# Optimization experiments

Hardware: AMD Instinct MI355X
Metric: run time of the kernel (lower is better)

The kernel has to match this reference:

```python
import jax, jax.numpy as jnp
import numpy as np

B, N, M, D = 2, 8192, 8192, 2
CIN, COUT, E, K = 32, 32, 16, 32
GAMMA = float(E * E)  # RBF sharpness
MUS = jnp.linspace(0.0, 1.0, E)  # RBF centers on [0, 1] (points drawn from unit square)


def setup_inputs() -> dict:
    key = jax.random.key(0)
    k1, k2, k3, k4, k5 = jax.random.split(key, 5)
    points_in = jax.random.uniform(k1, (B, N, D), dtype=jnp.float32)
    values_in = jax.random.normal(k2, (B, N, CIN), dtype=jnp.float32)
    points_out = jax.random.uniform(k3, (B, M, D), dtype=jnp.float32)
    coeff = jax.random.normal(k4, (CIN, COUT, E), dtype=jnp.float32)
    bias = jax.random.normal(k5, (COUT,), dtype=jnp.float32)
    return {"points_in": points_in, "values_in": values_in, "points_out": points_out,
            "coeff": coeff, "bias": bias}


def reference(points_in, values_in, points_out, coeff, bias):
    # u_inverse_v = g(points_out)^{-1} applied to points_in; for the translation
    # group this is the pairwise relative position tensor. Torch computes it
    # under no_grad -> stop_gradient here.
    uiv = points_out[:, :, None, :] - points_in[:, None, :, :]        # [B, M, N, D]
    norms = jnp.linalg.norm(uiv, axis=-1)                              # [B, M, N]
    neg_r, idx = jax.lax.top_k(-norms, K)                              # smallest K dists
    r_k = jax.lax.stop_gradient(-neg_r)                                # [B, M, K]
    idx = jax.lax.stop_gradient(idx)                                   # [B, M, K] int32
    uiv_k = jax.lax.stop_gradient(
        jnp.take_along_axis(uiv, idx[..., None], axis=2))              # [B, M, K, D]
    # det == 1 for translation group (non-Tensor in torch -> branch skipped)
    # gather neighbor values: values_in broadcast over M, gathered along N
    vals_k = jnp.take_along_axis(values_in[:, None, :, :], idx[..., None], axis=2)  # [B, M, K, CIN]
    # Gaussian radial kernel basis evaluated on |u_inverse_v|
    kernel_b = jnp.exp(-GAMMA * (r_k[..., None] - MUS) ** 2)           # [B, M, K, E]
    out = jnp.einsum('ioe,bmke,bmki->bmo', coeff, kernel_b, vals_k) / K
    out = out + bias
    return uiv_k, idx, out
```

## Files before the change

### kernel.cpp

```cpp
#include <hip/hip_runtime.h>
#include <cstdint>
#include <cstddef>

constexpr int BB   = 2;
constexpr int NN   = 8192;
constexpr int MM   = 8192;
constexpr int CIN  = 32;
constexpr int COUT = 32;
constexpr int EE   = 16;
constexpr int KK   = 32;
constexpr int GRID = 32;
constexpr int NCELL = GRID * GRID;

#define QPB 4
#define QPB2 8
#define CAP 128
#define KEY_BYTES 1040
#define VROW 36
#define VQS  1156
#define ECH 4

#define R0_FAST 0.0432f

constexpr size_t OFS_COEFFT = 0;
constexpr size_t OFS_COUNTS = 65536;
constexpr size_t OFS_CURSOR = 73728;
constexpr size_t OFS_STARTS = 81920;
constexpr size_t OFS_PTSS   = 90624;
constexpr size_t OFS_IDXS   = 221696;

__global__ __launch_bounds__(256) void prep_coeff_zero(const float* __restrict__ coeff,
                                                       float* __restrict__ coeff2,
                                                       int* __restrict__ cz) {
    int tid = blockIdx.x * 256 + threadIdx.x;
    if (tid < 2 * 2 * NCELL) cz[tid] = 0;
    if (tid >= EE * CIN * COUT) return;
    int o = tid & 31;
    int i = (tid >> 5) & 31;
    int e = tid >> 10;
    coeff2[tid] = coeff[(i * COUT + o) * EE + e];
}

__device__ __forceinline__ int cell_of(float2 p) {
    int cx = min(GRID - 1, max(0, (int)(p.x * (float)GRID)));
    int cy = min(GRID - 1, max(0, (int)(p.y * (float)GRID)));
    return cy * GRID + cx;
}

__global__ __launch_bounds__(256) void bin_count(const float* __restrict__ pts,
                                                 int* __restrict__ counts) {
    int t = blockIdx.x * 256 + threadIdx.x;
    int b = t >> 13, i = t & (NN - 1);
    float2 p = ((const float2*)pts)[(size_t)b * NN + i];
    atomicAdd(&counts[b * NCELL + cell_of(p)], 1);
}

__global__ __launch_bounds__(1024) void bin_scan(const int* __restrict__ counts,
                                                 int* __restrict__ starts) {
    __shared__ int wsum[16];
    const int b    = blockIdx.x;
    const int t    = threadIdx.x;
    const int lane = t & 63, wv = t >> 6;
    int s = counts[b * NCELL + t];
#pragma unroll
    for (int off = 1; off < 64; off <<= 1) {
        const int v = __shfl_up(s, off, 64);
        if (lane >= off) s += v;
    }
    if (lane == 63) wsum[wv] = s;
    __syncthreads();
    if (wv == 0) {
        int ws = (lane < 16) ? wsum[lane] : 0;
#pragma unroll
        for (int off = 1; off < 16; off <<= 1) {
            const int v = __shfl_up(ws, off, 64);
            if (lane >= off) ws += v;
        }
        if (lane < 16) wsum[lane] = ws;
    }
    __syncthreads();
    const int woff = (wv > 0) ? wsum[wv - 1] : 0;
    starts[b * (NCELL + 1) + t + 1] = s + woff;
    if (t == 0) starts[b * (NCELL + 1)] = 0;
}

__global__ __launch_bounds__(256) void bin_scatter(const float* __restrict__ pts,
                                                   const int* __restrict__ starts,
                                                   int* __restrict__ cursor,
                                                   float2* __restrict__ pts_s,
                                                   int* __restrict__ idx_s) {
    int t = blockIdx.x * 256 + threadIdx.x;
    int b = t >> 13, i = t & (NN - 1);
    float2 p = ((const float2*)pts)[(size_t)b * NN + i];
    int cell = cell_of(p);
    int pos = starts[b * (NCELL + 1) + cell] + atomicAdd(&cursor[b * NCELL + cell], 1);
    pts_s[(size_t)b * NN + pos] = p;
    idx_s[(size_t)b * NN + pos] = i;
}

__global__ __launch_bounds__(128) void conv_knn(
    const float2* __restrict__ pts_s, const int* __restrict__ idx_s,
    const int* __restrict__ starts,
    const float* __restrict__ points_in,
    const float* __restrict__ points_out,
    float* __restrict__ out_uiv, float* __restrict__ out_idx)
{
    __shared__ alignas(16) unsigned char SMEM[QPB][KEY_BYTES];

    const int tid   = threadIdx.x;
    const int sl    = tid & 31;
    const int qslot = tid >> 5;
    const int half  = qslot & 1;
    const int wid   = blockIdx.x * QPB + qslot;
    const int b     = wid >> 13;
    const int m     = wid & (MM - 1);

    unsigned long long* KEYq = (unsigned long long*)&SMEM[qslot][0];

    const float2* PS = pts_s + (size_t)b * NN;
    const int*    IS = idx_s + (size_t)b * NN;
    const int*    ST = starts + b * (NCELL + 1);
    const float2* P  = ((const float2*)points_in) + (size_t)b * NN;
    const float2  q  = ((const float2*)points_out)[(size_t)b * MM + m];

    const float INF = __builtin_inff();
    const float h = 1.0f / (float)GRID;
    const unsigned lmlt32 = (1u << sl) - 1u;

    float bd;
    int   bi;
    bool  ok = false;

    {
        float tau = R0_FAST;
        {
            const float bx = fminf(q.x, 1.0f - q.x);
            const float by = fminf(q.y, 1.0f - q.y);
#pragma unroll
            for (int it = 0; it < 3; ++it) {
                const float wx = 0.5f + 0.5f * fminf(bx / tau, 1.0f);
                const float wy = 0.5f + 0.5f * fminf(by / tau, 1.0f);
                tau = R0_FAST * __frsqrt_rn(wx * wy);
            }
        }
        const float tau2  = tau * tau;
        const float tau2a = tau2 * (1.0f + 2e-6f);

        const int xlo = (int)fmaxf((q.x - tau) * (float)GRID, 0.0f);
        const int xhi = (int)fminf((q.x + tau) * (float)GRID, (float)(GRID - 1));
        const int ylo = (int)fmaxf((q.y - tau) * (float)GRID, 0.0f);
        const int yhi = (int)fminf((q.y + tau) * (float)GRID, (float)(GRID - 1));
        const int nrows = yhi - ylo + 1;

        int sv = 0, ev = 0;
        if (sl < nrows) {
            sv = ST[(ylo + sl) * GRID + xlo];
            ev = ST[(ylo + sl) * GRID + xhi + 1];
        }

        int base = 0, nin = 0;
        for (int r = 0; r < nrows; ++r) {
            const int s = __shfl(sv, r, 32), e = __shfl(ev, r, 32);
            for (int j0 = s; j0 < e; j0 += 32) {
                const int j = j0 + sl;
                const bool valid = (j < e);
                float2 p = make_float2(2.0f, 2.0f);
                if (valid) p = PS[j];
                const float dx = q.x - p.x, dy = q.y - p.y;
                const float d2 = __builtin_fmaf(dy, dy, __fmul_rn(dx, dx));
                const bool adm = valid && (d2 <= tau2a);
                const unsigned bmA = (unsigned)(__ballot(adm) >> (half << 5));
                const unsigned bmS = (unsigned)(__ballot(valid && (d2 <= tau2)) >> (half << 5));
                nin += __popc(bmS);
                if (bmA) {
                    const float ex = __fsqrt_rn(__fadd_rn(__fmul_rn(dx, dx),
                                                          __fmul_rn(dy, dy)));
                    const int pos = base + __popc(bmA & lmlt32);
                    if (adm && pos < CAP)
                        KEYq[pos] =
                            ((unsigned long long)__float_as_uint(ex) << 32) | (unsigned)IS[j];
                    base += __popc(bmA);
                }
            }
        }

        ok = (nin >= 32) && (base <= CAP);
        if (ok) {
            unsigned long long k0 = (sl      < base) ? KEYq[sl]      : ~0ull;
            unsigned long long k1 = (sl + 32 < base) ? KEYq[sl + 32] : ~0ull;
            int r0 = 0, r1 = 0;
            if (!__any(base > 64)) {
                for (int t = 0; t < base; ++t) {
                    const unsigned long long kt = KEYq[t];
                    r0 += (kt < k0) ? 1 : 0;
                    r1 += (kt < k1) ? 1 : 0;
                }
            } else {
                unsigned long long k2 = (sl + 64 < base) ? KEYq[sl + 64] : ~0ull;
                unsigned long long k3 = (sl + 96 < base) ? KEYq[sl + 96] : ~0ull;
                int r2 = 0, r3 = 0;
                for (int t = 0; t < base; ++t) {
                    const unsigned long long kt = KEYq[t];
                    r0 += (kt < k0) ? 1 : 0;
                    r1 += (kt < k1) ? 1 : 0;
                    r2 += (kt < k2) ? 1 : 0;
                    r3 += (kt < k3) ? 1 : 0;
                }
                if (sl + 64 < base && r2 < 32) KEYq[r2] = k2;
                if (sl + 96 < base && r3 < 32) KEYq[r3] = k3;
            }
            if (sl      < base && r0 < 32) KEYq[r0] = k0;
            if (sl + 32 < base && r1 < 32) KEYq[r1] = k1;
            const unsigned long long kf = KEYq[sl];
            bd = __uint_as_float((unsigned)(kf >> 32));
            bi = (int)(unsigned)(kf & 0xffffffffull);

            const float tau32 = __shfl(bd, 31, 32);
            float g = INF;
            if (xlo > 0)        g = fminf(g, q.x - (float)xlo * h);
            if (xhi < GRID - 1) g = fminf(g, (float)(xhi + 1) * h - q.x);
            if (ylo > 0)        g = fminf(g, q.y - (float)ylo * h);
            if (yhi < GRID - 1) g = fminf(g, (float)(yhi + 1) * h - q.y);
            ok = (tau32 < g * (1.0f - 4e-6f));
        }
    }

    if (!ok) {
        const int cx = min(GRID - 1, max(0, (int)(q.x * (float)GRID)));
        const int cy = min(GRID - 1, max(0, (int)(q.y * (float)GRID)));
        int L = 2;
        for (;;) {
            const int xlo = max(cx - L, 0), xhi = min(cx + L, GRID - 1);
            const int ylo = max(cy - L, 0), yhi = min(cy + L, GRID - 1);
            const int nrows = yhi - ylo + 1;

            int sv = 0, ev = 0;
            if (sl < nrows) {
                sv = ST[(ylo + sl) * GRID + xlo];
                ev = ST[(ylo + sl) * GRID + xhi + 1];
            }

            float mn1 = INF, mn2 = INF;
            for (int r = 0; r < nrows; ++r) {
                const int s = __shfl(sv, r, 32), e = __shfl(ev, r, 32);
                for (int j = s + sl; j < e; j += 32) {
                    const float2 p = PS[j];
                    const float dx = q.x - p.x, dy = q.y - p.y;
                    const float d2 = __builtin_fmaf(dy, dy, __fmul_rn(dx, dx));
                    const float big = fmaxf(mn1, d2);
                    mn1 = fminf(mn1, d2);
                    mn2 = fminf(mn2, big);
                }
            }

            {
                float v = mn2;
#pragma unroll
                for (int k = 2; k <= 32; k <<= 1) {
#pragma unroll
                    for (int j = k >> 1; j > 0; j >>= 1) {
                        const float o = __shfl_xor(v, j, 32);
                        const bool up = ((sl & k) == 0), lower = ((sl & j) == 0);
                        const float mnv = fminf(v, o), mxv = fmaxf(v, o);
                        v = (lower == up) ? mnv : mxv;
                    }
                }
                mn2 = __shfl(v, 15, 32);
            }
            const float tau2b = mn2 * (1.0f + 4e-6f);

            int base = 0;
            for (int r = 0; r < nrows; ++r) {
                const int s = __shfl(sv, r, 32), e = __shfl(ev, r, 32);
                for (int j0 = s; j0 < e; j0 += 32) {
                    const int j = j0 + sl;
                    const bool valid = (j < e);
                    float2 p = make_float2(0.f, 0.f);
                    if (valid) p = PS[j];
                    const float dx = q.x - p.x, dy = q.y - p.y;
                    const float d2 = __builtin_fmaf(dy, dy, __fmul_rn(dx, dx));
                    const bool pred = valid && (d2 <= tau2b);
                    const unsigned bm = (unsigned)(__ballot(pred) >> (half << 5));
                    if (bm) {
                        const float ex = __fsqrt_rn(__fadd_rn(__fmul_rn(dx, dx),
                                                              __fmul_rn(dy, dy)));
                        const int pos = base + __popc(bm & lmlt32);
                        if (pred && pos < CAP)
                            KEYq[pos] =
                                ((unsigned long long)__float_as_uint(ex) << 32) | (unsigned)IS[j];
                        base += __popc(bm);
                    }
                }
            }

            if (base <= CAP) {
                unsigned long long k0 = (sl      < base) ? KEYq[sl]      : ~0ull;
                unsigned long long k1 = (sl + 32 < base) ? KEYq[sl + 32] : ~0ull;
                int r0 = 0, r1 = 0;
                if (!__any(base > 64)) {
                    for (int t = 0; t < base; ++t) {
                        const unsigned long long kt = KEYq[t];
                        r0 += (kt < k0) ? 1 : 0;
                        r1 += (kt < k1) ? 1 : 0;
                    }
                } else {
                    unsigned long long k2 = (sl + 64 < base) ? KEYq[sl + 64] : ~0ull;
                    unsigned long long k3 = (sl + 96 < base) ? KEYq[sl + 96] : ~0ull;
                    int r2 = 0, r3 = 0;
                    for (int t = 0; t < base; ++t) {
                        const unsigned long long kt = KEYq[t];
                        r0 += (kt < k0) ? 1 : 0;
                        r1 += (kt < k1) ? 1 : 0;
                        r2 += (kt < k2) ? 1 : 0;
                        r3 += (kt < k3) ? 1 : 0;
                    }
                    if (sl + 64 < base && r2 < 32) KEYq[r2] = k2;
                    if (sl + 96 < base && r3 < 32) KEYq[r3] = k3;
                }
                if (sl      < base && r0 < 32) KEYq[r0] = k0;
                if (sl + 32 < base && r1 < 32) KEYq[r1] = k1;
                if (base < 32 && sl >= base) KEYq[sl] = ~0ull;
                const unsigned long long kf = KEYq[sl];
                bd = __uint_as_float((unsigned)(kf >> 32));
                bi = (int)(unsigned)(kf & 0xffffffffull);
            } else {
                float fd = INF; int fi = 0x7FFFFFFF;
                for (int r = 0; r < nrows; ++r) {
                    const int s = __shfl(sv, r, 32), e = __shfl(ev, r, 32);
                    for (int j0 = s; j0 < e; j0 += 32) {
                        const int j = j0 + sl;
                        const bool valid = (j < e);
                        float2 p = make_float2(0.f, 0.f);
                        int vi0 = 0x7FFFFFFF;
                        if (valid) { p = PS[j]; vi0 = IS[j]; }
                        const float dx = q.x - p.x, dy = q.y - p.y;
                        const float d2 = __builtin_fmaf(dy, dy, __fmul_rn(dx, dx));
                        unsigned cm = (unsigned)(__ballot(valid && (d2 <= tau2b)) >> (half << 5));
                        const float ex = __fsqrt_rn(__fadd_rn(__fmul_rn(dx, dx),
                                                              __fmul_rn(dy, dy)));
                        while (cm) {
                            const int l = __builtin_ctz(cm); cm &= cm - 1;
                            const float v  = __shfl(ex, l, 32);
                            const int   vi = __shfl(vi0, l, 32);
                            const bool cl = (fd < v) || (fd == v && fi < vi);
                            const int pos = __popc((unsigned)(__ballot(cl) >> (half << 5)));
                            const float sd = __shfl_up(fd, 1, 32);
                            const int   si = __shfl_up(fi, 1, 32);
                            fd = (sl < pos) ? fd : ((sl == pos) ? v  : sd);
                            fi = (sl < pos) ? fi : ((sl == pos) ? vi : si);
                        }
                    }
                }
                bd = fd; bi = fi;
            }

            const float tau = __shfl(bd, 31, 32);
            float g = INF;
            if (xlo > 0)        g = fminf(g, q.x - (float)xlo * h);
            if (xhi < GRID - 1) g = fminf(g, (float)(xhi + 1) * h - q.x);
            if (ylo > 0)        g = fminf(g, q.y - (float)ylo * h);
            if (yhi < GRID - 1) g = fminf(g, (float)(yhi + 1) * h - q.y);
            if (tau < g * (1.0f - 4e-6f)) break;
            L += 2;
            if (L > GRID - 1) L = GRID - 1;
        }
    }

    {
        const float2 pk = P[bi];
        float2 u;
        u.x = q.x - pk.x;
        u.y = q.y - pk.y;
        ((float2*)out_uiv)[(size_t)wid * KK + sl] = u;
        out_idx[(size_t)wid * KK + sl] = (float)bi;
    }
}

__global__ __launch_bounds__(256) void conv_apply(
    const float* __restrict__ values_in,
    const float* __restrict__ out_uiv, const float* __restrict__ out_idx,
    const float* __restrict__ coeff2, const float* __restrict__ bias,
    float* __restrict__ out_val)
{
    __shared__ alignas(16) float VL[QPB2][VQS];
    __shared__ alignas(16) float CL[ECH][CIN][COUT];

    const int tid   = threadIdx.x;
    const int sl    = tid & 31;
    const int qslot = tid >> 5;
    const int wid   = blockIdx.x * QPB2 + qslot;
    const int b     = wid >> 13;

    float* VLq = &VL[qslot][0];

    const float2 u = ((const float2*)out_uiv)[(size_t)wid * KK + sl];
    const float bd = __fsqrt_rn(__fadd_rn(__fmul_rn(u.x, u.x), __fmul_rn(u.y, u.y)));
    const int   bi = (int)out_idx[(size_t)wid * KK + sl];

    {
        const float4* src = (const float4*)(values_in + ((size_t)b * NN + bi) * CIN);
        const float4 r0 = src[0], r1 = src[1], r2 = src[2], r3 = src[3];
        const float4 r4 = src[4], r5 = src[5], r6 = src[6], r7 = src[7];
        float4* dst = (float4*)(VLq + sl * VROW);
        dst[0] = r0; dst[1] = r1; dst[2] = r2; dst[3] = r3;
        dst[4] = r4; dst[5] = r5; dst[6] = r6; dst[7] = r7;
    }

    {
        const int e2 = sl >> 2;
        const int iq = sl & 3;
        const float mu0 = (float)(2 * e2)     * (1.0f / 15.0f);
        const float mu1 = (float)(2 * e2 + 1) * (1.0f / 15.0f);
        float4 A0a = make_float4(0.f, 0.f, 0.f, 0.f);
        float4 A0b = A0a, A1a = A0a, A1b = A0a;
#pragma unroll 8
        for (int k = 0; k < KK; ++k) {
            const float rk = __shfl(bd, k, 32);
            const float d0 = rk - mu0;
            const float d1 = rk - mu1;
            const float w0 = __expf(-256.0f * d0 * d0);
            const float w1 = __expf(-256.0f * d1 * d1);
            const float4* vr = (const float4*)(VLq + k * VROW + iq * 8);
            const float4 va = vr[0], vb = vr[1];
            A0a.x += w0 * va.x; A0a.y += w0 * va.y; A0a.z += w0 * va.z; A0a.w += w0 * va.w;
            A0b.x += w0 * vb.x; A0b.y += w0 * vb.y; A0b.z += w0 * vb.z; A0b.w += w0 * vb.w;
            A1a.x += w1 * va.x; A1a.y += w1 * va.y; A1a.z += w1 * va.z; A1a.w += w1 * va.w;
            A1b.x += w1 * vb.x; A1b.y += w1 * vb.y; A1b.z += w1 * vb.z; A1b.w += w1 * vb.w;
        }
        float4* t0 = (float4*)(VLq + (2 * e2)     * VROW + iq * 8);
        float4* t1 = (float4*)(VLq + (2 * e2 + 1) * VROW + iq * 8);
        t0[0] = A0a; t0[1] = A0b;
        t1[0] = A1a; t1[1] = A1b;
    }

    {
        const int w  = tid >> 6;
        const int rq = (tid >> 3) & 7;
        const int ro = tid & 7;
        float4 s4 = make_float4(0.f, 0.f, 0.f, 0.f);
        const float* Tq = &VL[rq][0];
#pragma unroll
        for (int ec = 0; ec < EE / ECH; ++ec) {
            __syncthreads();
            {
                const float4* src = (const float4*)(coeff2 + ec * (ECH * CIN * COUT));
                float4* dst = (float4*)&CL[0][0][0];
#pragma unroll
                for (int j = 0; j < (ECH * CIN * COUT) / (4 * 256); ++j) {
                    const int idx = tid + j * 256;
                    dst[idx] = src[idx];
                }
            }
            __syncthreads();
#pragma unroll
            for (int el = 0; el < ECH; ++el) {
                const int e = ec * ECH + el;
                const float* Trow = Tq + e * VROW + 8 * w;
                const float4 ta = *(const float4*)(Trow);
                const float4 tb = *(const float4*)(Trow + 4);
                const float* Crow = &CL[el][8 * w][0] + ro * 4;
#pragma unroll
                for (int ir = 0; ir < 4; ++ir) {
                    const float t = (ir == 0) ? ta.x : (ir == 1) ? ta.y
                                  : (ir == 2) ? ta.z : ta.w;
                    const float4 c = *(const float4*)(Crow + ir * COUT);
                    s4.x += t * c.x; s4.y += t * c.y;
                    s4.z += t * c.z; s4.w += t * c.w;
                }
#pragma unroll
                for (int ir = 0; ir < 4; ++ir) {
                    const float t = (ir == 0) ? tb.x : (ir == 1) ? tb.y
                                  : (ir == 2) ? tb.z : tb.w;
                    const float4 c = *(const float4*)(Crow + (4 + ir) * COUT);
                    s4.x += t * c.x; s4.y += t * c.y;
                    s4.z += t * c.z; s4.w += t * c.w;
                }
            }
        }
        __syncthreads();
        float4* PART = (float4*)&CL[0][0][0];
        PART[tid] = s4;
        __syncthreads();
        if (w == 0) {
            const float4 p0 = PART[tid];
            const float4 p1 = PART[tid + 64];
            const float4 p2 = PART[tid + 128];
            const float4 p3 = PART[tid + 192];
            const float4 bv = *(const float4*)(bias + ro * 4);
            float4 ov;
            ov.x = (p0.x + p1.x + p2.x + p3.x) * (1.0f / 32.0f) + bv.x;
            ov.y = (p0.y + p1.y + p2.y + p3.y) * (1.0f / 32.0f) + bv.y;
            ov.z = (p0.z + p1.z + p2.z + p3.z) * (1.0f / 32.0f) + bv.z;
            ov.w = (p0.w + p1.w + p2.w + p3.w) * (1.0f / 32.0f) + bv.w;
            const int qw = blockIdx.x * QPB2 + rq;
            *(float4*)(out_val + (size_t)qw * COUT + ro * 4) = ov;
        }
    }
}

extern "C" void kernel_launch(void* const* d_in, const int* in_sizes, int n_in,
                              void* d_out, int out_size, void* d_ws, size_t ws_size,
                              hipStream_t stream) {
    const float* points_in  = (const float*)d_in[0];
    const float* values_in  = (const float*)d_in[1];
    const float* points_out = (const float*)d_in[2];
    const float* coeff      = (const float*)d_in[3];
    const float* bias       = (const float*)d_in[4];

    float* out     = (float*)d_out;
    float* out_uiv = out;
    float* out_idx = out + (size_t)BB * MM * KK * 2;
    float* out_val = out_idx + (size_t)BB * MM * KK;

    char* ws = (char*)d_ws;
    float*  coeff2 = (float*)(ws + OFS_COEFFT);
    int*    counts = (int*)  (ws + OFS_COUNTS);
    int*    cursor = (int*)  (ws + OFS_CURSOR);
    int*    strts  = (int*)  (ws + OFS_STARTS);
    float2* pts_s  = (float2*)(ws + OFS_PTSS);
    int*    idx_s  = (int*)  (ws + OFS_IDXS);

    hipLaunchKernelGGL(prep_coeff_zero, dim3(64), dim3(256), 0, stream,
                       coeff, coeff2, counts);
    hipLaunchKernelGGL(bin_count, dim3(64), dim3(256), 0, stream, points_in, counts);
    hipLaunchKernelGGL(bin_scan, dim3(BB), dim3(1024), 0, stream, counts, strts);
    hipLaunchKernelGGL(bin_scatter, dim3(64), dim3(256), 0, stream,
                       points_in, strts, cursor, pts_s, idx_s);

    const int blocks1 = (BB * MM) / QPB;
    hipLaunchKernelGGL(conv_knn, dim3(blocks1), dim3(128), 0, stream,
                       pts_s, idx_s, strts, points_in, points_out,
                       out_uiv, out_idx);

    const int blocks2 = (BB * MM) / QPB2;
    hipLaunchKernelGGL(conv_apply, dim3(blocks2), dim3(256), 0, stream,
                       values_in, out_uiv, out_idx, coeff2, bias, out_val);
}
```

Baseline: 67.80 us.

## Fuse kNN search and convolution apply into one kernel

Merges the kNN search kernel and the convolution apply kernel into a single 256-thread kernel that handles 8 queries per block. The found neighbour index and distance stay in registers, so the output indices and offsets no longer have to be re-read from global memory, and one launch is removed. The kNN key scratch now shares an LDS region with the coefficient staging buffer. In exchange, blocks are larger, the search loop's divergence now co-exists with the apply phase's __syncthreads, and register and LDS pressure may reduce occupancy.

```diff
diff --git a/kernel.cpp b/kernel.cpp
--- a/kernel.cpp
+++ b/kernel.cpp
@@ -12,7 +12,6 @@
 constexpr int GRID = 32;
 constexpr int NCELL = GRID * GRID;
 
-#define QPB 4
 #define QPB2 8
 #define CAP 128
 #define KEY_BYTES 1040
@@ -98,24 +97,29 @@
     idx_s[(size_t)b * NN + pos] = i;
 }
 
-__global__ __launch_bounds__(128) void conv_knn(
+__global__ __launch_bounds__(256) void conv_fused(
     const float2* __restrict__ pts_s, const int* __restrict__ idx_s,
     const int* __restrict__ starts,
-    const float* __restrict__ points_in,
+    const float* __restrict__ points_in, const float* __restrict__ values_in,
     const float* __restrict__ points_out,
-    float* __restrict__ out_uiv, float* __restrict__ out_idx)
+    const float* __restrict__ coeff2, const float* __restrict__ bias,
+    float* __restrict__ out_uiv, float* __restrict__ out_idx,
+    float* __restrict__ out_val)
 {
-    __shared__ alignas(16) unsigned char SMEM[QPB][KEY_BYTES];
+    __shared__ alignas(16) float VL[QPB2][VQS];
+    __shared__ alignas(16) unsigned char CLRAW[ECH * CIN * COUT * 4];
 
     const int tid   = threadIdx.x;
     const int sl    = tid & 31;
     const int qslot = tid >> 5;
     const int half  = qslot & 1;
-    const int wid   = blockIdx.x * QPB + qslot;
+    const int wid   = blockIdx.x * QPB2 + qslot;
     const int b     = wid >> 13;
     const int m     = wid & (MM - 1);
 
-    unsigned long long* KEYq = (unsigned long long*)&SMEM[qslot][0];
+    unsigned long long* KEYq = (unsigned long long*)(CLRAW + qslot * KEY_BYTES);
+    float* CLf  = (float*)CLRAW;
+    float* VLq  = &VL[qslot][0];
 
     const float2* PS = pts_s + (size_t)b * NN;
     const int*    IS = idx_s + (size_t)b * NN;
@@ -374,28 +378,6 @@
         ((float2*)out_uiv)[(size_t)wid * KK + sl] = u;
         out_idx[(size_t)wid * KK + sl] = (float)bi;
     }
-}
-
-__global__ __launch_bounds__(256) void conv_apply(
-    const float* __restrict__ values_in,
-    const float* __restrict__ out_uiv, const float* __restrict__ out_idx,
-    const float* __restrict__ coeff2, const float* __restrict__ bias,
-    float* __restrict__ out_val)
-{
-    __shared__ alignas(16) float VL[QPB2][VQS];
-    __shared__ alignas(16) float CL[ECH][CIN][COUT];
-
-    const int tid   = threadIdx.x;
-    const int sl    = tid & 31;
-    const int qslot = tid >> 5;
-    const int wid   = blockIdx.x * QPB2 + qslot;
-    const int b     = wid >> 13;
-
-    float* VLq = &VL[qslot][0];
-
-    const float2 u = ((const float2*)out_uiv)[(size_t)wid * KK + sl];
-    const float bd = __fsqrt_rn(__fadd_rn(__fmul_rn(u.x, u.x), __fmul_rn(u.y, u.y)));
-    const int   bi = (int)out_idx[(size_t)wid * KK + sl];
 
     {
         const float4* src = (const float4*)(values_in + ((size_t)b * NN + bi) * CIN);
@@ -444,7 +426,7 @@
             __syncthreads();
             {
                 const float4* src = (const float4*)(coeff2 + ec * (ECH * CIN * COUT));
-                float4* dst = (float4*)&CL[0][0][0];
+                float4* dst = (float4*)CLRAW;
 #pragma unroll
                 for (int j = 0; j < (ECH * CIN * COUT) / (4 * 256); ++j) {
                     const int idx = tid + j * 256;
@@ -458,7 +440,7 @@
                 const float* Trow = Tq + e * VROW + 8 * w;
                 const float4 ta = *(const float4*)(Trow);
                 const float4 tb = *(const float4*)(Trow + 4);
-                const float* Crow = &CL[el][8 * w][0] + ro * 4;
+                const float* Crow = CLf + el * (CIN * COUT) + (8 * w) * COUT + ro * 4;
 #pragma unroll
                 for (int ir = 0; ir < 4; ++ir) {
                     const float t = (ir == 0) ? ta.x : (ir == 1) ? ta.y
@@ -478,7 +460,7 @@
             }
         }
         __syncthreads();
-        float4* PART = (float4*)&CL[0][0][0];
+        float4* PART = (float4*)CLRAW;
         PART[tid] = s4;
         __syncthreads();
         if (w == 0) {
@@ -527,12 +509,8 @@
     hipLaunchKernelGGL(bin_scatter, dim3(64), dim3(256), 0, stream,
                        points_in, strts, cursor, pts_s, idx_s);
 
-    const int blocks1 = (BB * MM) / QPB;
-    hipLaunchKernelGGL(conv_knn, dim3(blocks1), dim3(128), 0, stream,
-                       pts_s, idx_s, strts, points_in, points_out,
-                       out_uiv, out_idx);
-
-    const int blocks2 = (BB * MM) / QPB2;
-    hipLaunchKernelGGL(conv_apply, dim3(blocks2), dim3(256), 0, stream,
-                       values_in, out_uiv, out_idx, coeff2, bias, out_val);
-}
+    const int blocks = (BB * MM) / QPB2;
+    hipLaunchKernelGGL(conv_fused, dim3(blocks), dim3(256), 0, stream,
+                       pts_s, idx_s, strts, points_in, values_in, points_out,
+                       coeff2, bias, out_uiv, out_idx, out_val);
+}
```

After: 67.78 us. About the same (-0.0%).
